# Performance work log

Measured on AMD Instinct MI355X. Metric: run time of the kernel, lower is better.

Reference implementation:

```python
import jax, jax.numpy as jnp
import numpy as np

RATIO = 0.2
MIX_ALPHA = 0.5
TEMPERATURE = 0.1
EPS = 1e-12  # F.normalize eps


def setup_inputs() -> dict:
    key = jax.random.key(0)
    z = jax.random.normal(key, (16384, 256), dtype=jnp.float32)
    return {"z": z}


def reference(z):
    B = z.shape[0]
    n_hard = max(1, int(B * RATIO))

    # L2-normalize rows (F.normalize with eps clamp)
    norm = jnp.maximum(jnp.linalg.norm(z, axis=-1, keepdims=True), EPS)
    z_norm = z / norm

    # [B, B] cosine similarity, diagonal excluded
    sim = z_norm @ z_norm.T
    diag = jnp.eye(B, dtype=bool)
    sim = jnp.where(diag, -jnp.inf, sim)
    logits = sim / TEMPERATURE  # softmax(logits) == sim_probs

    # Batched sampling: replaces the per-sample Python loop with one fused pass
    key = jax.random.key(42)
    k_src, k_tgt, k_alpha = jax.random.split(key, 3)
    src_idx = jax.random.randint(k_src, (n_hard,), 0, B)  # torch.randint
    # categorical over logits rows == multinomial over softmax probs
    tgt_idx = jax.random.categorical(k_tgt, logits[src_idx], axis=-1)
    alpha = jax.random.uniform(k_alpha, (n_hard, 1), dtype=z.dtype) * MIX_ALPHA

    hard_negs = alpha * z[src_idx] + (1.0 - alpha) * z[tgt_idx]  # [n_hard, D]
    return hard_negs
```

## Files before the change

kernel.cpp:

```cpp
#include <hip/hip_runtime.h>
#include <stdint.h>
#include <math.h>

#define BN 16384
#define DK 256
#define NH 3276
#define NJB 26
#define NCB 128

typedef __attribute__((ext_vector_type(8))) short short8;
typedef __attribute__((ext_vector_type(4))) short short4v;
typedef __attribute__((ext_vector_type(4))) float f32x4;

__host__ __device__ __forceinline__ void tf2x32(uint32_t k0, uint32_t k1,
                                                uint32_t c0, uint32_t c1,
                                                uint32_t& o0, uint32_t& o1) {
  uint32_t ks2 = 0x1BD11BDAu ^ k0 ^ k1;
  uint32_t x0 = c0 + k0, x1 = c1 + k1;
#define RR(d) { x0 += x1; x1 = (x1 << d) | (x1 >> (32 - d)); x1 ^= x0; }
  RR(13) RR(15) RR(26) RR(6)   x0 += k1;  x1 += ks2 + 1u;
  RR(17) RR(29) RR(16) RR(24)  x0 += ks2; x1 += k0  + 2u;
  RR(13) RR(15) RR(26) RR(6)   x0 += k0;  x1 += k1  + 3u;
  RR(17) RR(29) RR(16) RR(24)  x0 += k1;  x1 += ks2 + 4u;
  RR(13) RR(15) RR(26) RR(6)   x0 += ks2; x1 += k0  + 5u;
#undef RR
  o0 = x0; o1 = x1;
}

__device__ __forceinline__ uint32_t rand32_at(uint32_t k0, uint32_t k1, uint32_t p) {
  uint32_t x0, x1; tf2x32(k0, k1, 0u, p, x0, x1);
  return x0 ^ x1;
}

__device__ __forceinline__ float unif01_from_bits(uint32_t bits) {
  return __uint_as_float((bits >> 9) | 0x3f800000u) - 1.0f;
}

__device__ __forceinline__ float gumbel_at(uint32_t k0, uint32_t k1, uint32_t p) {
  uint32_t bits = rand32_at(k0, k1, p);
  float f = unif01_from_bits(bits);
  float u = fmaxf(f, 1.17549435e-38f);
  float t = __log2f(u) * (-0.69314718055994531f);
  return __log2f(t) * (-0.69314718055994531f);
}

__device__ __forceinline__ unsigned long long packvc(float v, uint32_t c) {
  uint32_t u = __float_as_uint(v);
  u ^= ((int32_t)u < 0) ? 0xFFFFFFFFu : 0x80000000u;
  return ((unsigned long long)u << 32) | (unsigned long long)(~c);
}

__device__ __forceinline__ void glds16(const unsigned short* g, short* l) {
  __builtin_amdgcn_global_load_lds(
      (const __attribute__((address_space(1))) void*)g,
      (__attribute__((address_space(3))) void*)l, 16, 0, 0);
}

__global__ __launch_bounds__(256) void k_prep(const float* __restrict__ z,
                                              float* __restrict__ inv_norm,
                                              unsigned short* __restrict__ zh,
                                              unsigned short* __restrict__ zl,
                                              int* __restrict__ src_idx,
                                              unsigned long long* __restrict__ best,
                                              uint32_t k20, uint32_t k21) {
  int b = blockIdx.x, t = threadIdx.x;
  if (b < BN / 4) {
    int row = b * 4 + (t >> 6), lane = t & 63;
    float4 v = *(const float4*)&z[row * DK + lane * 4];
    float ss = v.x * v.x + v.y * v.y + v.z * v.z + v.w * v.w;
#pragma unroll
    for (int off = 32; off; off >>= 1) ss += __shfl_xor(ss, off, 64);
    if (lane == 0) inv_norm[row] = 1.0f / fmaxf(sqrtf(ss), 1e-12f);
    float f[4] = {v.x, v.y, v.z, v.w};
    short4v h, l;
#pragma unroll
    for (int i = 0; i < 4; ++i) {
      uint32_t u = __float_as_uint(f[i]);
      h[i] = (short)(u >> 16);
      float r = f[i] - __uint_as_float(u & 0xFFFF0000u);
      l[i] = (short)(__float_as_uint(r) >> 16);
    }
    *(short4v*)&zh[row * DK + lane * 4] = h;
    *(short4v*)&zl[row * DK + lane * 4] = l;
  } else {
    int i = (b - BN / 4) * 256 + t;
    if (i < NH) {
      uint32_t bits = rand32_at(k20, k21, (uint32_t)i);
      src_idx[i] = (int)(bits & (uint32_t)(BN - 1));
      best[i] = 0ull;
    }
  }
}

__global__ __launch_bounds__(256, 3) void k_main(const unsigned short* __restrict__ zh,
                                                 const unsigned short* __restrict__ zl,
                                                 const float* __restrict__ inv_norm,
                                                 const int* __restrict__ src_idx,
                                                 unsigned long long* __restrict__ best,
                                                 uint32_t kt0, uint32_t kt1) {
  __shared__ __align__(16) short As_hi[128 * 32];
  __shared__ __align__(16) short As_lo[128 * 32];
  __shared__ __align__(16) short Bs_hi[128 * 32];
  __shared__ __align__(16) short Bs_lo[128 * 32];

  const int flat = blockIdx.x;
  const int xcd = flat & 7, slot = flat >> 3;
  const int c_base = (xcd * 16 + (slot & 15)) * 128;
  const int j_base = (slot >> 4) * 128;

  const int t = threadIdx.x;
  const int lane = t & 63, w = t >> 6;

  const int r0 = w * 32 + (lane >> 2);
  const int r1 = r0 + 16;
  const int u0 = (lane & 3) ^ ((r0 >> 1) & 3);
  const int u1 = (lane & 3) ^ ((r1 >> 1) & 3);
  const int ga0 = src_idx[min(j_base + r0, NH - 1)];
  const int ga1 = src_idx[min(j_base + r1, NH - 1)];
  const uint32_t offA0 = (uint32_t)(ga0 * DK + u0 * 8);
  const uint32_t offA1 = (uint32_t)(ga1 * DK + u1 * 8);
  const uint32_t offB0 = (uint32_t)((c_base + r0) * DK + u0 * 8);
  const uint32_t offB1 = (uint32_t)((c_base + r1) * DK + u1 * 8);
  short* dA  = &As_hi[w * 1024];
  short* dAl = &As_lo[w * 1024];
  short* dB  = &Bs_hi[w * 1024];
  short* dBl = &Bs_lo[w * 1024];

  const int cl = lane & 15, q = lane >> 4;
  const int mb = (w >> 1) * 64 + cl;
  const int nb = (w & 1) * 64 + cl;

  f32x4 acc[4][4];
#pragma unroll
  for (int mt = 0; mt < 4; ++mt)
#pragma unroll
    for (int nt = 0; nt < 4; ++nt) acc[mt][nt] = (f32x4){0.f, 0.f, 0.f, 0.f};

#pragma unroll
  for (int kc = 0; kc < 8; ++kc) {
    const int ko = kc * 32;
    glds16(zh + offA0 + ko, dA);
    glds16(zh + offA1 + ko, dA + 512);
    glds16(zl + offA0 + ko, dAl);
    glds16(zl + offA1 + ko, dAl + 512);
    glds16(zh + offB0 + ko, dB);
    glds16(zh + offB1 + ko, dB + 512);
    glds16(zl + offB0 + ko, dBl);
    glds16(zl + offB1 + ko, dBl + 512);
    __syncthreads();

    short8 bh[4], bl[4];
#pragma unroll
    for (int nt = 0; nt < 4; ++nt) {
      int row = nb + nt * 16;
      int off = row * 32 + (q ^ ((row >> 1) & 3)) * 8;
      bh[nt] = *(const short8*)&Bs_hi[off];
      bl[nt] = *(const short8*)&Bs_lo[off];
    }
#pragma unroll
    for (int mt = 0; mt < 4; ++mt) {
      int row = mb + mt * 16;
      int off = row * 32 + (q ^ ((row >> 1) & 3)) * 8;
      short8 ah = *(const short8*)&As_hi[off];
      short8 al = *(const short8*)&As_lo[off];
#pragma unroll
      for (int nt = 0; nt < 4; ++nt) {
        acc[mt][nt] = __builtin_amdgcn_mfma_f32_16x16x32_bf16(ah, bh[nt], acc[mt][nt], 0, 0, 0);
        acc[mt][nt] = __builtin_amdgcn_mfma_f32_16x16x32_bf16(ah, bl[nt], acc[mt][nt], 0, 0, 0);
        acc[mt][nt] = __builtin_amdgcn_mfma_f32_16x16x32_bf16(al, bh[nt], acc[mt][nt], 0, 0, 0);
      }
    }
    __syncthreads();
  }

  const int q4 = (lane >> 4) * 4;
  const int coff = c_base + (w & 1) * 64;
  const int roff = j_base + (w >> 1) * 64;
  float invc[4]; int colg[4];
#pragma unroll
  for (int nt = 0; nt < 4; ++nt) {
    colg[nt] = coff + nt * 16 + cl;
    invc[nt] = inv_norm[colg[nt]];
  }
#pragma unroll
  for (int mt = 0; mt < 4; ++mt)
#pragma unroll
    for (int r = 0; r < 4; ++r) {
      int gj = roff + mt * 16 + q4 + r;
      int s = src_idx[min(gj, NH - 1)];
      float invs = inv_norm[s];
      uint32_t pbase = (uint32_t)gj * (uint32_t)BN;
      float bv = -INFINITY; uint32_t bc = 0;
#pragma unroll
      for (int nt = 0; nt < 4; ++nt) {
        float sim = acc[mt][nt][r] * invs * invc[nt];
        float gmb = gumbel_at(kt0, kt1, pbase + (uint32_t)colg[nt]);
        float tot = fmaf(sim, 10.0f, gmb);
        if (colg[nt] == s) tot = -INFINITY;
        if (tot > bv) { bv = tot; bc = (uint32_t)colg[nt]; }
      }
      unsigned long long key = packvc(bv, bc);
#pragma unroll
      for (int off = 1; off <= 8; off <<= 1) {
        unsigned long long o = __shfl_xor(key, off, 64);
        if (o > key) key = o;
      }
      if (cl == 0 && gj < NH) atomicMax(&best[gj], key);
    }
}

__global__ __launch_bounds__(64) void k_out(const float* __restrict__ z,
                                            const int* __restrict__ src_idx,
                                            const unsigned long long* __restrict__ best,
                                            float* __restrict__ out,
                                            uint32_t ka0, uint32_t ka1) {
  int j = blockIdx.x;
  int lane = threadIdx.x;
  int s = src_idx[j];
  int tgt = (int)(~((uint32_t)(best[j] & 0xFFFFFFFFull)));
  uint32_t bits = rand32_at(ka0, ka1, (uint32_t)j);
  float alpha = unif01_from_bits(bits) * 0.5f;
  float om = 1.0f - alpha;
  float4 a = *(const float4*)&z[s * DK + lane * 4];
  float4 b = *(const float4*)&z[tgt * DK + lane * 4];
  float4 o;
  o.x = alpha * a.x + om * b.x;
  o.y = alpha * a.y + om * b.y;
  o.z = alpha * a.z + om * b.z;
  o.w = alpha * a.w + om * b.w;
  *(float4*)&out[j * DK + lane * 4] = o;
}

extern "C" void kernel_launch(void* const* d_in, const int* in_sizes, int n_in,
                              void* d_out, int out_size, void* d_ws, size_t ws_size,
                              hipStream_t stream) {
  const float* z = (const float*)d_in[0];
  float* out = (float*)d_out;
  char* ws = (char*)d_ws;
  float*              inv_norm = (float*)(ws);
  int*                src_idx  = (int*)(ws + 65536);
  unsigned long long* best     = (unsigned long long*)(ws + 81920);
  unsigned short*     zh       = (unsigned short*)(ws + 131072);
  unsigned short*     zl       = (unsigned short*)(ws + 131072 + (size_t)BN * DK * 2);

  uint32_t r0 = 0u, r1 = 42u;
  uint32_t ks0, ks1, kt0, kt1, ka0, ka1, k20, k21;
  tf2x32(r0, r1, 0u, 0u, ks0, ks1);
  tf2x32(r0, r1, 0u, 1u, kt0, kt1);
  tf2x32(r0, r1, 0u, 2u, ka0, ka1);
  tf2x32(ks0, ks1, 0u, 1u, k20, k21);

  k_prep<<<dim3(BN / 4 + (NH + 255) / 256), dim3(256), 0, stream>>>(
      z, inv_norm, zh, zl, src_idx, best, k20, k21);
  k_main<<<dim3(NCB * NJB), dim3(256), 0, stream>>>(zh, zl, inv_norm, src_idx, best, kt0, kt1);
  k_out <<<dim3(NH), dim3(64), 0, stream>>>(z, src_idx, best, out, ka0, ka1);
}
```

Baseline: 267.2 us.

## Precompute Gumbel noise in separate kernel and pre-normalize rows before GEMM

When the workspace is large enough, the Gumbel noise (with the diagonal masked) is generated by a separate kernel into a ~213MB buffer. The GEMM kernel then reads it instead of computing Threefry hashes in its epilogue. Rows are also pre-normalized in the prep kernel, so the epilogue drops the inverse-norm multiplies, and the lean kernel allows higher occupancy. The trade is about 213MB written and then read back through HBM in place of ALU-heavy hashing, and the path depends on the available workspace size.

```diff
diff --git a/kernel.cpp b/kernel.cpp
--- a/kernel.cpp
+++ b/kernel.cpp
@@ -62,7 +62,8 @@
                                               unsigned short* __restrict__ zl,
                                               int* __restrict__ src_idx,
                                               unsigned long long* __restrict__ best,
-                                              uint32_t k20, uint32_t k21) {
+                                              uint32_t k20, uint32_t k21,
+                                              int normalize) {
   int b = blockIdx.x, t = threadIdx.x;
   if (b < BN / 4) {
     int row = b * 4 + (t >> 6), lane = t & 63;
@@ -70,8 +71,10 @@
     float ss = v.x * v.x + v.y * v.y + v.z * v.z + v.w * v.w;
 #pragma unroll
     for (int off = 32; off; off >>= 1) ss += __shfl_xor(ss, off, 64);
-    if (lane == 0) inv_norm[row] = 1.0f / fmaxf(sqrtf(ss), 1e-12f);
-    float f[4] = {v.x, v.y, v.z, v.w};
+    float inv = 1.0f / fmaxf(sqrtf(ss), 1e-12f);
+    if (lane == 0) inv_norm[row] = inv;
+    float s = normalize ? inv : 1.0f;
+    float f[4] = {v.x * s, v.y * s, v.z * s, v.w * s};
     short4v h, l;
 #pragma unroll
     for (int i = 0; i < 4; ++i) {
@@ -92,12 +95,29 @@
   }
 }
 
-__global__ __launch_bounds__(256, 3) void k_main(const unsigned short* __restrict__ zh,
-                                                 const unsigned short* __restrict__ zl,
-                                                 const float* __restrict__ inv_norm,
-                                                 const int* __restrict__ src_idx,
-                                                 unsigned long long* __restrict__ best,
-                                                 uint32_t kt0, uint32_t kt1) {
+__global__ __launch_bounds__(256) void k_gumbel(const int* __restrict__ src_idx,
+                                                float* __restrict__ g,
+                                                uint32_t kt0, uint32_t kt1) {
+  uint32_t p0 = (uint32_t)(blockIdx.x * 256 + threadIdx.x) * 8u;
+  int gj = (int)(p0 >> 14);
+  int c0 = (int)(p0 & 16383u);
+  int s = src_idx[min(gj, NH - 1)];
+  float o[8];
+#pragma unroll
+  for (int i = 0; i < 8; ++i) {
+    float gv = gumbel_at(kt0, kt1, p0 + (uint32_t)i);
+    o[i] = (c0 + i == s) ? -INFINITY : gv;
+  }
+  float4* dst = (float4*)&g[p0];
+  dst[0] = (float4){o[0], o[1], o[2], o[3]};
+  dst[1] = (float4){o[4], o[5], o[6], o[7]};
+}
+
+__global__ __launch_bounds__(256, 4) void k_main_lean(const unsigned short* __restrict__ zh,
+                                                      const unsigned short* __restrict__ zl,
+                                                      const float* __restrict__ g,
+                                                      const int* __restrict__ src_idx,
+                                                      unsigned long long* __restrict__ best) {
   __shared__ __align__(16) short As_hi[128 * 32];
   __shared__ __align__(16) short As_lo[128 * 32];
   __shared__ __align__(16) short Bs_hi[128 * 32];
@@ -176,6 +196,105 @@
   const int q4 = (lane >> 4) * 4;
   const int coff = c_base + (w & 1) * 64;
   const int roff = j_base + (w >> 1) * 64;
+#pragma unroll
+  for (int mt = 0; mt < 4; ++mt)
+#pragma unroll
+    for (int r = 0; r < 4; ++r) {
+      int gj = roff + mt * 16 + q4 + r;
+      const float* grow = g + (size_t)gj * BN + coff + cl;
+      float bv = -INFINITY; uint32_t bc = 0;
+#pragma unroll
+      for (int nt = 0; nt < 4; ++nt) {
+        float gv = grow[nt * 16];
+        float tot = fmaf(acc[mt][nt][r], 10.0f, gv);
+        if (tot > bv) { bv = tot; bc = (uint32_t)(coff + nt * 16 + cl); }
+      }
+      unsigned long long key = packvc(bv, bc);
+#pragma unroll
+      for (int off = 1; off <= 8; off <<= 1) {
+        unsigned long long o = __shfl_xor(key, off, 64);
+        if (o > key) key = o;
+      }
+      if (cl == 0 && gj < NH) atomicMax(&best[gj], key);
+    }
+}
+
+__global__ __launch_bounds__(256, 3) void k_main_fused(const unsigned short* __restrict__ zh,
+                                                       const unsigned short* __restrict__ zl,
+                                                       const float* __restrict__ inv_norm,
+                                                       const int* __restrict__ src_idx,
+                                                       unsigned long long* __restrict__ best,
+                                                       uint32_t kt0, uint32_t kt1) {
+  __shared__ __align__(16) short As_hi[128 * 32];
+  __shared__ __align__(16) short As_lo[128 * 32];
+  __shared__ __align__(16) short Bs_hi[128 * 32];
+  __shared__ __align__(16) short Bs_lo[128 * 32];
+  const int flat = blockIdx.x;
+  const int xcd = flat & 7, slot = flat >> 3;
+  const int c_base = (xcd * 16 + (slot & 15)) * 128;
+  const int j_base = (slot >> 4) * 128;
+  const int t = threadIdx.x;
+  const int lane = t & 63, w = t >> 6;
+  const int r0 = w * 32 + (lane >> 2);
+  const int r1 = r0 + 16;
+  const int u0 = (lane & 3) ^ ((r0 >> 1) & 3);
+  const int u1 = (lane & 3) ^ ((r1 >> 1) & 3);
+  const int ga0 = src_idx[min(j_base + r0, NH - 1)];
+  const int ga1 = src_idx[min(j_base + r1, NH - 1)];
+  const uint32_t offA0 = (uint32_t)(ga0 * DK + u0 * 8);
+  const uint32_t offA1 = (uint32_t)(ga1 * DK + u1 * 8);
+  const uint32_t offB0 = (uint32_t)((c_base + r0) * DK + u0 * 8);
+  const uint32_t offB1 = (uint32_t)((c_base + r1) * DK + u1 * 8);
+  short* dA  = &As_hi[w * 1024];
+  short* dAl = &As_lo[w * 1024];
+  short* dB  = &Bs_hi[w * 1024];
+  short* dBl = &Bs_lo[w * 1024];
+  const int cl = lane & 15, q = lane >> 4;
+  const int mb = (w >> 1) * 64 + cl;
+  const int nb = (w & 1) * 64 + cl;
+  f32x4 acc[4][4];
+#pragma unroll
+  for (int mt = 0; mt < 4; ++mt)
+#pragma unroll
+    for (int nt = 0; nt < 4; ++nt) acc[mt][nt] = (f32x4){0.f, 0.f, 0.f, 0.f};
+#pragma unroll
+  for (int kc = 0; kc < 8; ++kc) {
+    const int ko = kc * 32;
+    glds16(zh + offA0 + ko, dA);
+    glds16(zh + offA1 + ko, dA + 512);
+    glds16(zl + offA0 + ko, dAl);
+    glds16(zl + offA1 + ko, dAl + 512);
+    glds16(zh + offB0 + ko, dB);
+    glds16(zh + offB1 + ko, dB + 512);
+    glds16(zl + offB0 + ko, dBl);
+    glds16(zl + offB1 + ko, dBl + 512);
+    __syncthreads();
+    short8 bh[4], bl[4];
+#pragma unroll
+    for (int nt = 0; nt < 4; ++nt) {
+      int row = nb + nt * 16;
+      int off = row * 32 + (q ^ ((row >> 1) & 3)) * 8;
+      bh[nt] = *(const short8*)&Bs_hi[off];
+      bl[nt] = *(const short8*)&Bs_lo[off];
+    }
+#pragma unroll
+    for (int mt = 0; mt < 4; ++mt) {
+      int row = mb + mt * 16;
+      int off = row * 32 + (q ^ ((row >> 1) & 3)) * 8;
+      short8 ah = *(const short8*)&As_hi[off];
+      short8 al = *(const short8*)&As_lo[off];
+#pragma unroll
+      for (int nt = 0; nt < 4; ++nt) {
+        acc[mt][nt] = __builtin_amdgcn_mfma_f32_16x16x32_bf16(ah, bh[nt], acc[mt][nt], 0, 0, 0);
+        acc[mt][nt] = __builtin_amdgcn_mfma_f32_16x16x32_bf16(ah, bl[nt], acc[mt][nt], 0, 0, 0);
+        acc[mt][nt] = __builtin_amdgcn_mfma_f32_16x16x32_bf16(al, bh[nt], acc[mt][nt], 0, 0, 0);
+      }
+    }
+    __syncthreads();
+  }
+  const int q4 = (lane >> 4) * 4;
+  const int coff = c_base + (w & 1) * 64;
+  const int roff = j_base + (w >> 1) * 64;
   float invc[4]; int colg[4];
 #pragma unroll
   for (int nt = 0; nt < 4; ++nt) {
@@ -194,8 +313,10 @@
 #pragma unroll
       for (int nt = 0; nt < 4; ++nt) {
         float sim = acc[mt][nt][r] * invs * invc[nt];
-        float gmb = gumbel_at(kt0, kt1, pbase + (uint32_t)colg[nt]);
-        float tot = fmaf(sim, 10.0f, gmb);
+        float gmb = gumbel_at(0u, 0u, 0u);
+        (void)gmb;
+        float gv = gumbel_at(kt0, kt1, pbase + (uint32_t)colg[nt]);
+        float tot = fmaf(sim, 10.0f, gv);
         if (colg[nt] == s) tot = -INFINITY;
         if (tot > bv) { bv = tot; bc = (uint32_t)colg[nt]; }
       }
@@ -237,11 +358,14 @@
   const float* z = (const float*)d_in[0];
   float* out = (float*)d_out;
   char* ws = (char*)d_ws;
-  float*              inv_norm = (float*)(ws);
-  int*                src_idx  = (int*)(ws + 65536);
-  unsigned long long* best     = (unsigned long long*)(ws + 81920);
+  int*                src_idx  = (int*)(ws);
+  unsigned long long* best     = (unsigned long long*)(ws + 16384);
+  float*              inv_norm = (float*)(ws + 49152);
   unsigned short*     zh       = (unsigned short*)(ws + 131072);
-  unsigned short*     zl       = (unsigned short*)(ws + 131072 + (size_t)BN * DK * 2);
+  unsigned short*     zl       = (unsigned short*)(ws + 131072 + 8388608);
+  float*              gbuf     = (float*)(ws + 131072 + 2 * 8388608);
+  const size_t need_g = 131072 + 2 * 8388608 + (size_t)3328 * BN * 4;
+  const bool use_g = ws_size >= need_g;
 
   uint32_t r0 = 0u, r1 = 42u;
   uint32_t ks0, ks1, kt0, kt1, ka0, ka1, k20, k21;
@@ -251,7 +375,12 @@
   tf2x32(ks0, ks1, 0u, 1u, k20, k21);
 
   k_prep<<<dim3(BN / 4 + (NH + 255) / 256), dim3(256), 0, stream>>>(
-      z, inv_norm, zh, zl, src_idx, best, k20, k21);
-  k_main<<<dim3(NCB * NJB), dim3(256), 0, stream>>>(zh, zl, inv_norm, src_idx, best, kt0, kt1);
-  k_out <<<dim3(NH), dim3(64), 0, stream>>>(z, src_idx, best, out, ka0, ka1);
-}
+      z, inv_norm, zh, zl, src_idx, best, k20, k21, use_g ? 1 : 0);
+  if (use_g) {
+    k_gumbel<<<dim3(3328 * BN / (256 * 8)), dim3(256), 0, stream>>>(src_idx, gbuf, kt0, kt1);
+    k_main_lean<<<dim3(NCB * NJB), dim3(256), 0, stream>>>(zh, zl, gbuf, src_idx, best);
+  } else {
+    k_main_fused<<<dim3(NCB * NJB), dim3(256), 0, stream>>>(zh, zl, inv_norm, src_idx, best, kt0, kt1);
+  }
+  k_out<<<dim3(NH), dim3(64), 0, stream>>>(z, src_idx, best, out, ka0, ka1);
+}
```

Measured after the change: 354.7 us. 32.7% more time.
